# Kernel optimization log

Measured on AMD Instinct MI355X. Metric: run time of the kernel, lower is better.

The kernel has to match this reference:

```python
import jax, jax.numpy as jnp
import numpy as np

C_M, C_Z = 256, 128
MIN_BIN, MAX_BIN, NO_BINS = 3.25, 20.75, 15
INF = 1e8
EPS = 1e-5
N_RES = 768


def _layer_norm(t, gamma, beta):
    mu = jnp.mean(t, axis=-1, keepdims=True)
    var = jnp.var(t, axis=-1, keepdims=True)
    return (t - mu) * jax.lax.rsqrt(var + EPS) * gamma + beta


def setup_inputs() -> dict:
    key = jax.random.key(0)
    ks = jax.random.split(key, 5)
    m = jax.random.normal(ks[0], (1, N_RES, C_M), dtype=jnp.float32)
    z = jax.random.normal(ks[1], (1, N_RES, N_RES, C_Z), dtype=jnp.float32)
    # coordinates in Angstrom-ish scale so distances span the bins
    x = jax.random.normal(ks[2], (1, N_RES, 3), dtype=jnp.float32) * 10.0
    w_lin = jax.random.normal(ks[3], (C_Z, NO_BINS), dtype=jnp.float32) * (1.0 / np.sqrt(NO_BINS))
    b_lin = jnp.zeros((C_Z,), dtype=jnp.float32)
    g_m = jnp.ones((C_M,), dtype=jnp.float32)
    be_m = jnp.zeros((C_M,), dtype=jnp.float32)
    g_z = jnp.ones((C_Z,), dtype=jnp.float32)
    be_z = jnp.zeros((C_Z,), dtype=jnp.float32)
    return {"m": m, "z": z, "x": x, "w_lin": w_lin, "b_lin": b_lin,
            "g_m": g_m, "be_m": be_m, "g_z": g_z, "be_z": be_z}


def reference(m, z, x, w_lin, b_lin, g_m, be_m, g_z, be_z):
    bins = jnp.linspace(MIN_BIN, MAX_BIN, NO_BINS, dtype=x.dtype)
    sq_bins = bins ** 2                                   # [no_bins]
    upper = jnp.concatenate([sq_bins[1:], jnp.array([INF], dtype=x.dtype)])

    m_update = _layer_norm(m, g_m, be_m)                  # [*, N, C_m]

    # squared pairwise distances [*, N, N, 1]
    d2 = jnp.sum((x[..., None, :] - x[..., None, :, :]) ** 2, axis=-1, keepdims=True)
    # one-hot distogram [*, N, N, no_bins]
    oh = ((d2 > sq_bins) & (d2 < upper)).astype(x.dtype)
    # linear embed: [*, N, N, c_z]
    d_emb = jnp.einsum('...b,cb->...c', oh, w_lin) + b_lin

    z_update = d_emb + _layer_norm(z, g_z, be_z)
    return m_update, z_update
```

## Files before the change

### kernel.cpp

```cpp
#include <hip/hip_runtime.h>

#define N_RES 768
#define C_M 256
#define C_Z 128
#define NO_BINS 15

__global__ __launch_bounds__(256) void prep_kernel(const float* __restrict__ w_lin,
                                                   const float* __restrict__ b_lin,
                                                   const float* __restrict__ be_z,
                                                   float* __restrict__ ws) {
    const int tid = threadIdx.x;
    for (int idx = tid; idx < NO_BINS * C_Z; idx += 256) {
        const int c = idx / NO_BINS;
        const int b = idx - c * NO_BINS;
        ws[b * C_Z + c] = w_lin[idx];
    }
    if (tid < C_Z) {
        ws[NO_BINS * C_Z + tid] = be_z[tid] + b_lin[tid];
    }
}

__global__ __launch_bounds__(64) void ln_m_kernel(const float* __restrict__ m,
                                                  const float* __restrict__ g,
                                                  const float* __restrict__ b,
                                                  float* __restrict__ out) {
    const int row  = blockIdx.x;
    const int lane = threadIdx.x;
    const float4 v = ((const float4*)(m + row * C_M))[lane];
    float s  = v.x + v.y + v.z + v.w;
    float ss = v.x * v.x + v.y * v.y + v.z * v.z + v.w * v.w;
#pragma unroll
    for (int off = 32; off >= 1; off >>= 1) {
        s  += __shfl_xor(s,  off);
        ss += __shfl_xor(ss, off);
    }
    const float mu  = s * (1.0f / C_M);
    const float var = ss * (1.0f / C_M) - mu * mu;
    const float rs  = rsqrtf(var + 1e-5f);
    const float4 gv = ((const float4*)g)[lane];
    const float4 bv = ((const float4*)b)[lane];
    float4 o;
    o.x = (v.x - mu) * rs * gv.x + bv.x;
    o.y = (v.y - mu) * rs * gv.y + bv.y;
    o.z = (v.z - mu) * rs * gv.z + bv.z;
    o.w = (v.w - mu) * rs * gv.w + bv.w;
    ((float4*)(out + row * C_M))[lane] = o;
}

__global__ __launch_bounds__(256) void z_fused_kernel(const float* __restrict__ z,
                                                      const float* __restrict__ x,
                                                      const float* __restrict__ ws,
                                                      const float* __restrict__ g_z,
                                                      float* __restrict__ out) {
    const int tid  = threadIdx.x;
    const int half = tid >> 5;
    const int hl   = tid & 31;
    const int row  = blockIdx.x * 8 + half;
    const int i    = row / N_RES;
    const int j    = row - i * N_RES;

    const float dx = x[i * 3 + 0] - x[j * 3 + 0];
    const float dy = x[i * 3 + 1] - x[j * 3 + 1];
    const float dz = x[i * 3 + 2] - x[j * 3 + 2];
    const float d2 = __fadd_rn(__fadd_rn(__fmul_rn(dx, dx), __fmul_rn(dy, dy)),
                               __fmul_rn(dz, dz));

    int bin = -1;
#pragma unroll
    for (int b = 0; b < NO_BINS; b++) {
        const float lov = 3.25f + 1.25f * (float)b;
        const float hiv = 3.25f + 1.25f * (float)(b + 1);
        const float lo  = lov * lov;
        const float hi  = (b < NO_BINS - 1) ? hiv * hiv : 1e8f;
        if (d2 > lo && d2 < hi) bin = b;
    }

    const float4 v = ((const float4*)(z + (size_t)row * C_Z))[hl];
    float s  = v.x + v.y + v.z + v.w;
    float ss = v.x * v.x + v.y * v.y + v.z * v.z + v.w * v.w;
#pragma unroll
    for (int off = 16; off >= 1; off >>= 1) {
        s  += __shfl_xor(s,  off);
        ss += __shfl_xor(ss, off);
    }
    const float mu  = s * (1.0f / C_Z);
    const float var = ss * (1.0f / C_Z) - mu * mu;
    const float rs  = rsqrtf(var + 1e-5f);

    const float4 gv = ((const float4*)g_z)[hl];
    const float4 bv = ((const float4*)(ws + NO_BINS * C_Z))[hl];
    float4 wv = make_float4(0.f, 0.f, 0.f, 0.f);
    if (bin >= 0) wv = ((const float4*)(ws + bin * C_Z))[hl];

    float4 o;
    o.x = (v.x - mu) * rs * gv.x + bv.x + wv.x;
    o.y = (v.y - mu) * rs * gv.y + bv.y + wv.y;
    o.z = (v.z - mu) * rs * gv.z + bv.z + wv.z;
    o.w = (v.w - mu) * rs * gv.w + bv.w + wv.w;
    ((float4*)(out + (size_t)row * C_Z))[hl] = o;
}

extern "C" void kernel_launch(void* const* d_in, const int* in_sizes, int n_in,
                              void* d_out, int out_size, void* d_ws, size_t ws_size,
                              hipStream_t stream) {
    const float* m     = (const float*)d_in[0];
    const float* z     = (const float*)d_in[1];
    const float* x     = (const float*)d_in[2];
    const float* w_lin = (const float*)d_in[3];
    const float* b_lin = (const float*)d_in[4];
    const float* g_m   = (const float*)d_in[5];
    const float* be_m  = (const float*)d_in[6];
    const float* g_z   = (const float*)d_in[7];
    const float* be_z  = (const float*)d_in[8];

    float* out   = (float*)d_out;
    float* out_m = out;
    float* out_z = out + N_RES * C_M;
    float* ws    = (float*)d_ws;

    prep_kernel<<<1, 256, 0, stream>>>(w_lin, b_lin, be_z, ws);
    ln_m_kernel<<<N_RES, 64, 0, stream>>>(m, g_m, be_m, out_m);

    const int n_rows = N_RES * N_RES;
    z_fused_kernel<<<n_rows / 8, 256, 0, stream>>>(z, x, ws, g_z, out_z);
}
```

Measured before the change: 497.4 us.

## Fuse m layer-norm into z kernel and process 16 rows per block

Merges the separate m layer-norm launch into the z kernel by appending extra blocks that handle m rows, removing one kernel launch. Each z row is now handled by 16 lanes with two float4 loads each instead of 32 lanes with one, so a block covers 16 rows and the shuffle reduction has one fewer step. This raises per-thread work and memory-level parallelism but changes the coalescing pattern, and the kernel stays bound by memory bandwidth.

```diff
diff --git a/kernel.cpp b/kernel.cpp
--- a/kernel.cpp
+++ b/kernel.cpp
@@ -4,6 +4,9 @@
 #define C_M 256
 #define C_Z 128
 #define NO_BINS 15
+#define Z_ROWS (N_RES * N_RES)
+#define Z_BLOCKS (Z_ROWS / 16)
+#define M_BLOCKS (N_RES / 16)
 
 __global__ __launch_bounds__(256) void prep_kernel(const float* __restrict__ w_lin,
                                                    const float* __restrict__ b_lin,
@@ -20,84 +23,136 @@
     }
 }
 
-__global__ __launch_bounds__(64) void ln_m_kernel(const float* __restrict__ m,
-                                                  const float* __restrict__ g,
-                                                  const float* __restrict__ b,
-                                                  float* __restrict__ out) {
-    const int row  = blockIdx.x;
-    const int lane = threadIdx.x;
-    const float4 v = ((const float4*)(m + row * C_M))[lane];
-    float s  = v.x + v.y + v.z + v.w;
-    float ss = v.x * v.x + v.y * v.y + v.z * v.z + v.w * v.w;
+__global__ __launch_bounds__(256) void fused_kernel(const float* __restrict__ z,
+                                                    const float* __restrict__ x,
+                                                    const float* __restrict__ ws,
+                                                    const float* __restrict__ g_z,
+                                                    const float* __restrict__ m,
+                                                    const float* __restrict__ g_m,
+                                                    const float* __restrict__ be_m,
+                                                    float* __restrict__ out_z,
+                                                    float* __restrict__ out_m) {
+    const int tid = threadIdx.x;
+    const int grp = tid >> 4;
+    const int hl  = tid & 15;
+
+    if (blockIdx.x < Z_BLOCKS) {
+        const int row = blockIdx.x * 16 + grp;
+        const int i   = row / N_RES;
+        const int j   = row - i * N_RES;
+
+        const float dx = x[i * 3 + 0] - x[j * 3 + 0];
+        const float dy = x[i * 3 + 1] - x[j * 3 + 1];
+        const float dz = x[i * 3 + 2] - x[j * 3 + 2];
+        const float d2 = __fadd_rn(__fadd_rn(__fmul_rn(dx, dx), __fmul_rn(dy, dy)),
+                                   __fmul_rn(dz, dz));
+
+        int bin = -1;
 #pragma unroll
-    for (int off = 32; off >= 1; off >>= 1) {
-        s  += __shfl_xor(s,  off);
-        ss += __shfl_xor(ss, off);
+        for (int b = 0; b < NO_BINS; b++) {
+            const float lov = 3.25f + 1.25f * (float)b;
+            const float hiv = 3.25f + 1.25f * (float)(b + 1);
+            const float lo  = lov * lov;
+            const float hi  = (b < NO_BINS - 1) ? hiv * hiv : 1e8f;
+            if (d2 > lo && d2 < hi) bin = b;
+        }
+
+        const float4* zr = (const float4*)(z + (size_t)row * C_Z);
+        const float4 v0 = zr[hl];
+        const float4 v1 = zr[hl + 16];
+
+        float s  = ((v0.x + v0.y) + (v0.z + v0.w)) + ((v1.x + v1.y) + (v1.z + v1.w));
+        float ss = (v0.x * v0.x + v0.y * v0.y + v0.z * v0.z + v0.w * v0.w)
+                 + (v1.x * v1.x + v1.y * v1.y + v1.z * v1.z + v1.w * v1.w);
+#pragma unroll
+        for (int off = 8; off >= 1; off >>= 1) {
+            s  += __shfl_xor(s,  off);
+            ss += __shfl_xor(ss, off);
+        }
+        const float mu  = s * (1.0f / C_Z);
+        const float var = ss * (1.0f / C_Z) - mu * mu;
+        const float rs  = rsqrtf(var + 1e-5f);
+
+        const float4 gv0 = ((const float4*)g_z)[hl];
+        const float4 gv1 = ((const float4*)g_z)[hl + 16];
+        const float4 bv0 = ((const float4*)(ws + NO_BINS * C_Z))[hl];
+        const float4 bv1 = ((const float4*)(ws + NO_BINS * C_Z))[hl + 16];
+        float4 wv0 = make_float4(0.f, 0.f, 0.f, 0.f);
+        float4 wv1 = make_float4(0.f, 0.f, 0.f, 0.f);
+        if (bin >= 0) {
+            wv0 = ((const float4*)(ws + bin * C_Z))[hl];
+            wv1 = ((const float4*)(ws + bin * C_Z))[hl + 16];
+        }
+
+        float4 o0, o1;
+        o0.x = (v0.x - mu) * rs * gv0.x + bv0.x + wv0.x;
+        o0.y = (v0.y - mu) * rs * gv0.y + bv0.y + wv0.y;
+        o0.z = (v0.z - mu) * rs * gv0.z + bv0.z + wv0.z;
+        o0.w = (v0.w - mu) * rs * gv0.w + bv0.w + wv0.w;
+        o1.x = (v1.x - mu) * rs * gv1.x + bv1.x + wv1.x;
+        o1.y = (v1.y - mu) * rs * gv1.y + bv1.y + wv1.y;
+        o1.z = (v1.z - mu) * rs * gv1.z + bv1.z + wv1.z;
+        o1.w = (v1.w - mu) * rs * gv1.w + bv1.w + wv1.w;
+
+        float4* orow = (float4*)(out_z + (size_t)row * C_Z);
+        orow[hl]      = o0;
+        orow[hl + 16] = o1;
+    } else {
+        const int row = (blockIdx.x - Z_BLOCKS) * 16 + grp;
+        const float4* mr = (const float4*)(m + row * C_M);
+        const float4 v0 = mr[hl];
+        const float4 v1 = mr[hl + 16];
+        const float4 v2 = mr[hl + 32];
+        const float4 v3 = mr[hl + 48];
+
+        float s  = ((v0.x + v0.y) + (v0.z + v0.w)) + ((v1.x + v1.y) + (v1.z + v1.w))
+                 + ((v2.x + v2.y) + (v2.z + v2.w)) + ((v3.x + v3.y) + (v3.z + v3.w));
+        float ss = (v0.x * v0.x + v0.y * v0.y + v0.z * v0.z + v0.w * v0.w)
+                 + (v1.x * v1.x + v1.y * v1.y + v1.z * v1.z + v1.w * v1.w)
+                 + (v2.x * v2.x + v2.y * v2.y + v2.z * v2.z + v2.w * v2.w)
+                 + (v3.x * v3.x + v3.y * v3.y + v3.z * v3.z + v3.w * v3.w);
+#pragma unroll
+        for (int off = 8; off >= 1; off >>= 1) {
+            s  += __shfl_xor(s,  off);
+            ss += __shfl_xor(ss, off);
+        }
+        const float mu  = s * (1.0f / C_M);
+        const float var = ss * (1.0f / C_M) - mu * mu;
+        const float rs  = rsqrtf(var + 1e-5f);
+
+        const float4 g0 = ((const float4*)g_m)[hl];
+        const float4 g1 = ((const float4*)g_m)[hl + 16];
+        const float4 g2 = ((const float4*)g_m)[hl + 32];
+        const float4 g3 = ((const float4*)g_m)[hl + 48];
+        const float4 b0 = ((const float4*)be_m)[hl];
+        const float4 b1 = ((const float4*)be_m)[hl + 16];
+        const float4 b2 = ((const float4*)be_m)[hl + 32];
+        const float4 b3 = ((const float4*)be_m)[hl + 48];
+
+        float4 o0, o1, o2, o3;
+        o0.x = (v0.x - mu) * rs * g0.x + b0.x;
+        o0.y = (v0.y - mu) * rs * g0.y + b0.y;
+        o0.z = (v0.z - mu) * rs * g0.z + b0.z;
+        o0.w = (v0.w - mu) * rs * g0.w + b0.w;
+        o1.x = (v1.x - mu) * rs * g1.x + b1.x;
+        o1.y = (v1.y - mu) * rs * g1.y + b1.y;
+        o1.z = (v1.z - mu) * rs * g1.z + b1.z;
+        o1.w = (v1.w - mu) * rs * g1.w + b1.w;
+        o2.x = (v2.x - mu) * rs * g2.x + b2.x;
+        o2.y = (v2.y - mu) * rs * g2.y + b2.y;
+        o2.z = (v2.z - mu) * rs * g2.z + b2.z;
+        o2.w = (v2.w - mu) * rs * g2.w + b2.w;
+        o3.x = (v3.x - mu) * rs * g3.x + b3.x;
+        o3.y = (v3.y - mu) * rs * g3.y + b3.y;
+        o3.z = (v3.z - mu) * rs * g3.z + b3.z;
+        o3.w = (v3.w - mu) * rs * g3.w + b3.w;
+
+        float4* orow = (float4*)(out_m + row * C_M);
+        orow[hl]      = o0;
+        orow[hl + 16] = o1;
+        orow[hl + 32] = o2;
+        orow[hl + 48] = o3;
     }
-    const float mu  = s * (1.0f / C_M);
-    const float var = ss * (1.0f / C_M) - mu * mu;
-    const float rs  = rsqrtf(var + 1e-5f);
-    const float4 gv = ((const float4*)g)[lane];
-    const float4 bv = ((const float4*)b)[lane];
-    float4 o;
-    o.x = (v.x - mu) * rs * gv.x + bv.x;
-    o.y = (v.y - mu) * rs * gv.y + bv.y;
-    o.z = (v.z - mu) * rs * gv.z + bv.z;
-    o.w = (v.w - mu) * rs * gv.w + bv.w;
-    ((float4*)(out + row * C_M))[lane] = o;
-}
-
-__global__ __launch_bounds__(256) void z_fused_kernel(const float* __restrict__ z,
-                                                      const float* __restrict__ x,
-                                                      const float* __restrict__ ws,
-                                                      const float* __restrict__ g_z,
-                                                      float* __restrict__ out) {
-    const int tid  = threadIdx.x;
-    const int half = tid >> 5;
-    const int hl   = tid & 31;
-    const int row  = blockIdx.x * 8 + half;
-    const int i    = row / N_RES;
-    const int j    = row - i * N_RES;
-
-    const float dx = x[i * 3 + 0] - x[j * 3 + 0];
-    const float dy = x[i * 3 + 1] - x[j * 3 + 1];
-    const float dz = x[i * 3 + 2] - x[j * 3 + 2];
-    const float d2 = __fadd_rn(__fadd_rn(__fmul_rn(dx, dx), __fmul_rn(dy, dy)),
-                               __fmul_rn(dz, dz));
-
-    int bin = -1;
-#pragma unroll
-    for (int b = 0; b < NO_BINS; b++) {
-        const float lov = 3.25f + 1.25f * (float)b;
-        const float hiv = 3.25f + 1.25f * (float)(b + 1);
-        const float lo  = lov * lov;
-        const float hi  = (b < NO_BINS - 1) ? hiv * hiv : 1e8f;
-        if (d2 > lo && d2 < hi) bin = b;
-    }
-
-    const float4 v = ((const float4*)(z + (size_t)row * C_Z))[hl];
-    float s  = v.x + v.y + v.z + v.w;
-    float ss = v.x * v.x + v.y * v.y + v.z * v.z + v.w * v.w;
-#pragma unroll
-    for (int off = 16; off >= 1; off >>= 1) {
-        s  += __shfl_xor(s,  off);
-        ss += __shfl_xor(ss, off);
-    }
-    const float mu  = s * (1.0f / C_Z);
-    const float var = ss * (1.0f / C_Z) - mu * mu;
-    const float rs  = rsqrtf(var + 1e-5f);
-
-    const float4 gv = ((const float4*)g_z)[hl];
-    const float4 bv = ((const float4*)(ws + NO_BINS * C_Z))[hl];
-    float4 wv = make_float4(0.f, 0.f, 0.f, 0.f);
-    if (bin >= 0) wv = ((const float4*)(ws + bin * C_Z))[hl];
-
-    float4 o;
-    o.x = (v.x - mu) * rs * gv.x + bv.x + wv.x;
-    o.y = (v.y - mu) * rs * gv.y + bv.y + wv.y;
-    o.z = (v.z - mu) * rs * gv.z + bv.z + wv.z;
-    o.w = (v.w - mu) * rs * gv.w + bv.w + wv.w;
-    ((float4*)(out + (size_t)row * C_Z))[hl] = o;
 }
 
 extern "C" void kernel_launch(void* const* d_in, const int* in_sizes, int n_in,
@@ -119,8 +174,7 @@
     float* ws    = (float*)d_ws;
 
     prep_kernel<<<1, 256, 0, stream>>>(w_lin, b_lin, be_z, ws);
-    ln_m_kernel<<<N_RES, 64, 0, stream>>>(m, g_m, be_m, out_m);
-
-    const int n_rows = N_RES * N_RES;
-    z_fused_kernel<<<n_rows / 8, 256, 0, stream>>>(z, x, ws, g_z, out_z);
+    fused_kernel<<<Z_BLOCKS + M_BLOCKS, 256, 0, stream>>>(z, x, ws, g_z,
+                                                          m, g_m, be_m,
+                                                          out_z, out_m);
 }
```

Result: no change. 497.8 us (+0.1%).
